# Kernel optimization log

Measured on AMD Instinct MI355X. Metric: run time of the kernel, lower is better.

## Reference

```python
import jax, jax.numpy as jnp
import numpy as np

B, N, T, D, H = 2, 1024, 12, 64, 4
HD = D // H


def _ln(x, g, b, eps=1e-5):
    m = x.mean(-1, keepdims=True)
    v = x.var(-1, keepdims=True)
    return (x - m) / jnp.sqrt(v + eps) * g + b


def setup_inputs() -> dict:
    key = jax.random.key(0)
    ks = jax.random.split(key, 12)
    s = 1.0 / np.sqrt(D)
    s4 = 1.0 / np.sqrt(4 * D)
    return {
        "x": jax.random.normal(ks[0], (B, N, T, D), jnp.float32),
        "adj": jax.random.randint(ks[1], (N, N), 0, 2, jnp.int32),
        "wq": jax.random.normal(ks[2], (D, D), jnp.float32) * s,
        "wk": jax.random.normal(ks[3], (D, D), jnp.float32) * s,
        "wv": jax.random.normal(ks[4], (D, D), jnp.float32) * s,
        "wo": jax.random.normal(ks[5], (D, D), jnp.float32) * s,
        "bo": jnp.zeros((D,), jnp.float32),
        "w1": jax.random.normal(ks[6], (D, 4 * D), jnp.float32) * s,
        "b1": jnp.zeros((4 * D,), jnp.float32),
        "w2": jax.random.normal(ks[7], (4 * D, D), jnp.float32) * s4,
        "b2": jnp.zeros((D,), jnp.float32),
        "g1": jnp.ones((D,), jnp.float32),
        "be1": jnp.zeros((D,), jnp.float32),
        "g2": jnp.ones((D,), jnp.float32),
        "be2": jnp.zeros((D,), jnp.float32),
    }


def reference(x, adj, wq, wk, wv, wo, bo, w1, b1, w2, b2, g1, be1, g2, be2):
    # x: [B, N, T, D]; all timesteps are independent -> vectorize over T.
    b, n, t, d = x.shape
    xt = x.transpose(0, 2, 1, 3)  # [B, T, N, D]
    h = _ln(xt, g1, be1)
    q = (h @ wq).reshape(b, t, n, H, HD)
    k = (h @ wk).reshape(b, t, n, H, HD)
    v = (h @ wv).reshape(b, t, n, H, HD)
    # scores: [B, T, H, N, N]
    scores = jnp.einsum("btihc,btjhc->bthij", q, k) / np.sqrt(HD)
    scores = jnp.where(adj[None, None, None] == 0, jnp.float32(-1e9), scores)
    attn = jax.nn.softmax(scores, axis=-1)
    o = jnp.einsum("bthij,btjhc->btihc", attn, v).reshape(b, t, n, d)
    xt = xt + (o @ wo + bo)
    h = _ln(xt, g2, be2)
    h = jax.nn.relu(h @ w1 + b1) @ w2 + b2
    xt = xt + h
    return xt.transpose(0, 2, 1, 3)  # [B, N, T, D]
```

## Files before the change

### kernel.cpp

```cpp
#include <hip/hip_runtime.h>
#include <hip/hip_bf16.h>

#define DEV __device__ __forceinline__

constexpr int Nn = 1024, Tn = 12, Dn = 64;

#if __has_builtin(__builtin_amdgcn_exp2f)
DEV float fast_exp2(float x) { return __builtin_amdgcn_exp2f(x); }
#else
DEV float fast_exp2(float x) { return exp2f(x); }
#endif

typedef __bf16 bf16x8 __attribute__((ext_vector_type(8)));
typedef float f32x4 __attribute__((ext_vector_type(4)));
typedef float f32x16 __attribute__((ext_vector_type(16)));

#define Z16 {0.f,0.f,0.f,0.f, 0.f,0.f,0.f,0.f, 0.f,0.f,0.f,0.f, 0.f,0.f,0.f,0.f}

DEV unsigned f2b(float f) {
  unsigned u = __builtin_bit_cast(unsigned, f);
  return (u + 0x8000u) >> 16;
}
DEV unsigned pk2(float a, float b) { return f2b(a) | (f2b(b) << 16); }
DEV float b2f(unsigned hbits) { return __builtin_bit_cast(float, hbits << 16); }
DEV void split2(float a, float b, unsigned& hw, unsigned& lw) {
  unsigned ha = f2b(a), hb = f2b(b);
  hw = ha | (hb << 16);
  lw = pk2(a - b2f(ha), b - b2f(hb));
}

DEV void wave_reduce2(float& s, float& s2) {
#pragma unroll
  for (int off = 32; off; off >>= 1) {
    s += __shfl_xor(s, off, 64);
    s2 += __shfl_xor(s2, off, 64);
  }
}

__global__ __launch_bounds__(256) void k_pack(const int* __restrict__ adj,
                                              unsigned long long* __restrict__ packed) {
  int gw = (blockIdx.x * 256 + threadIdx.x) >> 6;
  int lane = threadIdx.x & 63;
  int v = adj[(gw << 6) + lane];
  unsigned long long m = __ballot(v != 0);
  if (lane == 0) packed[gw] = m;
}

__global__ __launch_bounds__(256) void k_prep(
    const float* __restrict__ wo, const float* __restrict__ w1,
    const float* __restrict__ w2, const float* __restrict__ b1,
    const float* __restrict__ g2, const float* __restrict__ be2,
    __hip_bfloat16* __restrict__ woP, __hip_bfloat16* __restrict__ w1P,
    __hip_bfloat16* __restrict__ w2P, float* __restrict__ b1p) {
  int tid = blockIdx.x * 256 + threadIdx.x;
  if (tid < 512) {
    int fg = tid >> 6, lane = tid & 63;
    int t = fg >> 2, ks = fg & 3, hi = lane >> 5, l31 = lane & 31;
    unsigned hw[4], lw[4];
#pragma unroll
    for (int jj = 0; jj < 4; ++jj) {
      int k = ks * 16 + hi * 8 + jj * 2;
      split2(wo[k * 64 + t * 32 + l31], wo[(k + 1) * 64 + t * 32 + l31], hw[jj], lw[jj]);
    }
    *(uint4*)(woP + (size_t)tid * 8) = make_uint4(hw[0], hw[1], hw[2], hw[3]);
    *(uint4*)(woP + (size_t)(512 + tid) * 8) = make_uint4(lw[0], lw[1], lw[2], lw[3]);
  } else if (tid < 2560) {
    int id = tid - 512;
    int fg = id >> 6, lane = id & 63;
    int tile = fg >> 2, ks = fg & 3, hi = lane >> 5, l31 = lane & 31;
    unsigned hw[4], lw[4];
#pragma unroll
    for (int jj = 0; jj < 4; ++jj) {
      int k = ks * 16 + hi * 8 + jj * 2;
      split2(g2[k] * w1[k * 256 + tile * 32 + l31],
             g2[k + 1] * w1[(k + 1) * 256 + tile * 32 + l31], hw[jj], lw[jj]);
    }
    *(uint4*)(w1P + (size_t)id * 8) = make_uint4(hw[0], hw[1], hw[2], hw[3]);
    *(uint4*)(w1P + (size_t)(2048 + id) * 8) = make_uint4(lw[0], lw[1], lw[2], lw[3]);
  } else if (tid < 4608) {
    int id = tid - 2560;
    int fg = id >> 6, lane = id & 63;
    int t = fg >> 4, ks = fg & 15, hi = lane >> 5, l31 = lane & 31;
    unsigned hw[4], lw[4];
#pragma unroll
    for (int jj = 0; jj < 4; ++jj) {
      int k = ks * 16 + hi * 8 + jj * 2;
      split2(w2[k * 64 + t * 32 + l31], w2[(k + 1) * 64 + t * 32 + l31], hw[jj], lw[jj]);
    }
    *(uint4*)(w2P + (size_t)id * 8) = make_uint4(hw[0], hw[1], hw[2], hw[3]);
    *(uint4*)(w2P + (size_t)(2048 + id) * 8) = make_uint4(lw[0], lw[1], lw[2], lw[3]);
  } else if (tid < 4864) {
    int o = tid - 4608;
    float s = b1[o];
    for (int c = 0; c < 64; ++c) s += be2[c] * w1[c * 256 + o];
    b1p[o] = s;
  }
}

__global__ __launch_bounds__(256) void k_ln1_qkv(
    const float* __restrict__ x, const float* __restrict__ wq,
    const float* __restrict__ wk, const float* __restrict__ wv,
    const float* __restrict__ g1, const float* __restrict__ be1,
    __hip_bfloat16* __restrict__ Qb, __hip_bfloat16* __restrict__ Kb,
    __hip_bfloat16* __restrict__ Vt) {
  __shared__ float wlds[64 * 192];
  __shared__ float hlds[4][16][68];
  int tid = threadIdx.x, lane = tid & 63, w = tid >> 6;
  for (int i = tid * 4; i < 4096; i += 1024) {
    int c = i >> 6, d = i & 63;
    *(float4*)&wlds[c * 192 + d]       = *(const float4*)&wq[i];
    *(float4*)&wlds[c * 192 + 64 + d]  = *(const float4*)&wk[i];
    *(float4*)&wlds[c * 192 + 128 + d] = *(const float4*)&wv[i];
  }
  float g = g1[lane], be = be1[lane];
  __syncthreads();
  int row0 = blockIdx.x * 64 + w * 16;
  int bt = row0 >> 10, n0 = row0 & 1023;
#pragma unroll 1
  for (int r = 0; r < 16; ++r) {
    int n = n0 + r;
    int b = bt / Tn, t = bt - b * Tn;
    float xv = x[((b * Nn + n) * Tn + t) * 64 + lane];
    float s = xv, s2 = xv * xv;
    wave_reduce2(s, s2);
    float mean = s * 0.015625f;
    float var = s2 * 0.015625f - mean * mean;
    float rs = rsqrtf(var + 1e-5f);
    hlds[w][r][lane] = (xv - mean) * rs * g + be;
  }
  float qa[16], ka[16], va[16];
#pragma unroll
  for (int r = 0; r < 16; ++r) { qa[r] = 0.f; ka[r] = 0.f; va[r] = 0.f; }
  for (int c = 0; c < 64; c += 4) {
    float wq4[4], wk4[4], wv4[4];
#pragma unroll
    for (int cc = 0; cc < 4; ++cc) {
      wq4[cc] = wlds[(c + cc) * 192 + lane];
      wk4[cc] = wlds[(c + cc) * 192 + 64 + lane];
      wv4[cc] = wlds[(c + cc) * 192 + 128 + lane];
    }
#pragma unroll
    for (int r = 0; r < 16; ++r) {
      float4 h4 = *(float4*)&hlds[w][r][c];
      qa[r] = fmaf(h4.x, wq4[0], qa[r]); qa[r] = fmaf(h4.y, wq4[1], qa[r]);
      qa[r] = fmaf(h4.z, wq4[2], qa[r]); qa[r] = fmaf(h4.w, wq4[3], qa[r]);
      ka[r] = fmaf(h4.x, wk4[0], ka[r]); ka[r] = fmaf(h4.y, wk4[1], ka[r]);
      ka[r] = fmaf(h4.z, wk4[2], ka[r]); ka[r] = fmaf(h4.w, wk4[3], ka[r]);
      va[r] = fmaf(h4.x, wv4[0], va[r]); va[r] = fmaf(h4.y, wv4[1], va[r]);
      va[r] = fmaf(h4.z, wv4[2], va[r]); va[r] = fmaf(h4.w, wv4[3], va[r]);
    }
  }
  const float QS = 0.25f * 1.44269504088896f;
  int hh = lane >> 4, cc = lane & 15;
#pragma unroll 1
  for (int r = 0; r < 16; ++r) {
    int n = n0 + r;
    size_t idx = ((size_t)(bt * 4 + hh) * 1024 + n) * 16 + cc;
    Qb[idx] = __hip_bfloat16_raw{(unsigned short)f2b(qa[r] * QS)};
    Kb[idx] = __hip_bfloat16_raw{(unsigned short)f2b(ka[r])};
  }
#pragma unroll
  for (int r = 0; r < 16; ++r) hlds[w][r][lane] = va[r];
  unsigned os[8];
#pragma unroll
  for (int j = 0; j < 8; ++j)
    os[j] = f2b(hlds[w][2 * j][lane]) | (f2b(hlds[w][2 * j + 1][lane]) << 16);
  uint4* vo = (uint4*)(Vt + ((size_t)(bt * 4 + hh) * 16 + cc) * 1024 + n0);
  vo[0] = make_uint4(os[0], os[1], os[2], os[3]);
  vo[1] = make_uint4(os[4], os[5], os[6], os[7]);
}

__global__ __launch_bounds__(256) void k_attn(
    const __hip_bfloat16* __restrict__ Qb, const __hip_bfloat16* __restrict__ Kb,
    const __hip_bfloat16* __restrict__ Vt, const unsigned* __restrict__ packed32,
    float* __restrict__ O) {
  __shared__ uint4 smem[4][160];
  int bid = (blockIdx.x & 7) * 96 + (blockIdx.x >> 3);
  int bth = bid >> 3, qb = bid & 7;
  int bt = bth >> 2, h = bth & 3;
  int tid = threadIdx.x, lane = tid & 63, w = tid >> 6;
  int l15 = lane & 15, l31 = lane & 31, hi = lane >> 5, g4 = lane >> 4;
  int q0 = qb * 128 + w * 32;
  bf16x8 qfrag = __builtin_bit_cast(bf16x8,
      *(const uint4*)(Qb + ((size_t)bth * 1024 + q0 + l31) * 16 + hi * 8));
  const uint4* kbase = (const uint4*)(Kb + (size_t)bth * 1024 * 16);
  const uint4* vtb = (const uint4*)(Vt + (size_t)bth * 16 * 1024);
  const unsigned* mbase = packed32 + (size_t)(q0 + l31) * 32;
  char* myp = (char*)&smem[w][0];

  f32x4 o1 = {0.f, 0.f, 0.f, 0.f}, o2 = {0.f, 0.f, 0.f, 0.f};
  float m = -1e38f, lsum = 0.f;
  uint4 kf = kbase[l31 * 2 + hi];
  uint4 vf = vtb[l15 * 128 + g4];
  unsigned mk = mbase[0];
#pragma unroll 1
  for (int kt = 0; kt < 32; ++kt) {
    int ktn = kt < 31 ? kt + 1 : 31;
    uint4 kf_n = kbase[ktn * 64 + l31 * 2 + hi];
    uint4 vf_n = vtb[l15 * 128 + ktn * 4 + g4];
    unsigned mk_n = mbase[ktn];
    f32x16 s = Z16;
    s = __builtin_amdgcn_mfma_f32_32x32x16_bf16(
        __builtin_bit_cast(bf16x8, kf), qfrag, s, 0, 0, 0);
    unsigned mm = mk >> (hi * 4);
#pragma unroll
    for (int r = 0; r < 16; ++r)
      if (!((mm >> ((r & 3) + 8 * (r >> 2))) & 1u)) s[r] = -3e38f;
    float tm = s[0];
#pragma unroll
    for (int r = 1; r < 16; ++r) tm = fmaxf(tm, s[r]);
    tm = fmaxf(tm, __shfl_xor(tm, 32));
    float mn = fmaxf(m, tm);
    float sc = fast_exp2(m - mn);
    m = mn;
    lsum *= sc;
    float sc1 = __shfl(sc, l15), sc2 = __shfl(sc, l15 + 16);
#pragma unroll
    for (int r = 0; r < 4; ++r) { o1[r] *= sc1; o2[r] *= sc2; }
    float p[16];
#pragma unroll
    for (int r = 0; r < 16; ++r) { p[r] = fast_exp2(s[r] - m); lsum += p[r]; }
    unsigned pw[8];
#pragma unroll
    for (int j = 0; j < 8; ++j) pw[j] = pk2(p[2 * j], p[2 * j + 1]);
    char* wp = myp + l31 * 80 + hi * 8;
    *(uint2*)(wp +  0) = make_uint2(pw[0], pw[1]);
    *(uint2*)(wp + 16) = make_uint2(pw[2], pw[3]);
    *(uint2*)(wp + 32) = make_uint2(pw[4], pw[5]);
    *(uint2*)(wp + 48) = make_uint2(pw[6], pw[7]);
    uint4 b1v = *(uint4*)(myp + l15 * 80 + g4 * 16);
    uint4 b2v = *(uint4*)(myp + (l15 + 16) * 80 + g4 * 16);
    bf16x8 vfrag = __builtin_bit_cast(bf16x8, vf);
    o1 = __builtin_amdgcn_mfma_f32_16x16x32_bf16(
        vfrag, __builtin_bit_cast(bf16x8, b1v), o1, 0, 0, 0);
    o2 = __builtin_amdgcn_mfma_f32_16x16x32_bf16(
        vfrag, __builtin_bit_cast(bf16x8, b2v), o2, 0, 0, 0);
    kf = kf_n; vf = vf_n; mk = mk_n;
  }
  float lt = lsum + __shfl_xor(lsum, 32);
  float inv = lt > 0.f ? 1.f / lt : 0.f;
  float inv1 = __shfl(inv, l15), inv2 = __shfl(inv, l15 + 16);
  float* of = (float*)myp;
#pragma unroll
  for (int r = 0; r < 4; ++r) {
    of[l15 * 20 + g4 * 4 + r] = o1[r] * inv1;
    of[(l15 + 16) * 20 + g4 * 4 + r] = o2[r] * inv2;
  }
  float* orow = O + ((size_t)bt * 1024 + q0 + l31) * 64 + h * 16 + hi * 8;
  *(float4*)(orow)     = *(float4*)(myp + l31 * 80 + hi * 32);
  *(float4*)(orow + 4) = *(float4*)(myp + l31 * 80 + hi * 32 + 16);
}

__global__ __launch_bounds__(64) void k_tail(
    const float* __restrict__ O, const float* __restrict__ x,
    const __hip_bfloat16* __restrict__ woP, const __hip_bfloat16* __restrict__ w1P,
    const __hip_bfloat16* __restrict__ w2P, const float* __restrict__ bo,
    const float* __restrict__ b1p, const float* __restrict__ b2,
    float* __restrict__ out) {
  __shared__ float bias[384];
  __shared__ char wbuf[13312];
  int lane = threadIdx.x & 63;
  int l31 = lane & 31, hi = lane >> 5;
  for (int i = threadIdx.x; i < 384; i += 64)
    bias[i] = i < 64 ? bo[i] : (i < 128 ? b2[i - 64] : b1p[i - 128]);
  __syncthreads();

  int tok = blockIdx.x * 32 + l31;
  int bt = tok >> 10, n = tok & 1023;
  int b = bt / Tn, tt_time = bt - b * Tn;
  const float* orow = O + (size_t)tok * 64;
  const float* xrow = x + ((size_t)(b * Nn + n) * Tn + tt_time) * 64;
  char* h2b = wbuf;
  char* pub = wbuf + 8704;

#define LDA(base, g) __builtin_bit_cast(bf16x8, *(const uint4*)((base) + ((size_t)(g) * 64 + lane) * 8))
#define MF(A, B, C) __builtin_amdgcn_mfma_f32_32x32x16_bf16(A, B, C, 0, 0, 0)

  bf16x8 ofh[4], ofl[4];
#pragma unroll
  for (int ks = 0; ks < 4; ++ks) {
    float4 oa = *(const float4*)(orow + ks * 16 + hi * 8);
    float4 ob = *(const float4*)(orow + ks * 16 + hi * 8 + 4);
    unsigned hw[4], lw[4];
    split2(oa.x, oa.y, hw[0], lw[0]); split2(oa.z, oa.w, hw[1], lw[1]);
    split2(ob.x, ob.y, hw[2], lw[2]); split2(ob.z, ob.w, hw[3], lw[3]);
    ofh[ks] = __builtin_bit_cast(bf16x8, make_uint4(hw[0], hw[1], hw[2], hw[3]));
    ofl[ks] = __builtin_bit_cast(bf16x8, make_uint4(lw[0], lw[1], lw[2], lw[3]));
  }
  f32x16 d1a = Z16, d1b = Z16;
#pragma unroll
  for (int ks = 0; ks < 4; ++ks) {
    bf16x8 wha = LDA(woP, ks), wla = LDA(woP, 8 + ks);
    d1a = MF(wha, ofh[ks], d1a); d1a = MF(wha, ofl[ks], d1a); d1a = MF(wla, ofh[ks], d1a);
    bf16x8 whb = LDA(woP, 4 + ks), wlb = LDA(woP, 12 + ks);
    d1b = MF(whb, ofh[ks], d1b); d1b = MF(whb, ofl[ks], d1b); d1b = MF(wlb, ofh[ks], d1b);
  }
#pragma unroll
  for (int rq = 0; rq < 4; ++rq) {
    float4 xa = *(const float4*)(xrow + rq * 8 + hi * 4);
    float4 xb = *(const float4*)(xrow + 32 + rq * 8 + hi * 4);
    int ca = rq * 8 + hi * 4, cb = 32 + rq * 8 + hi * 4;
    d1a[rq * 4 + 0] += bias[ca + 0] + xa.x;  d1a[rq * 4 + 1] += bias[ca + 1] + xa.y;
    d1a[rq * 4 + 2] += bias[ca + 2] + xa.z;  d1a[rq * 4 + 3] += bias[ca + 3] + xa.w;
    d1b[rq * 4 + 0] += bias[cb + 0] + xb.x;  d1b[rq * 4 + 1] += bias[cb + 1] + xb.y;
    d1b[rq * 4 + 2] += bias[cb + 2] + xb.z;  d1b[rq * 4 + 3] += bias[cb + 3] + xb.w;
  }
  float s = 0.f, s2 = 0.f;
#pragma unroll
  for (int r = 0; r < 16; ++r) {
    s += d1a[r] + d1b[r];
    s2 += d1a[r] * d1a[r] + d1b[r] * d1b[r];
  }
  s += __shfl_xor(s, 32);  s2 += __shfl_xor(s2, 32);
  float mean = s * 0.015625f;
  float rs = rsqrtf(s2 * 0.015625f - mean * mean + 1e-5f);
#pragma unroll
  for (int rq = 0; rq < 4; ++rq) {
    unsigned h0, l0, h1, l1;
    split2((d1a[rq * 4 + 0] - mean) * rs, (d1a[rq * 4 + 1] - mean) * rs, h0, l0);
    split2((d1a[rq * 4 + 2] - mean) * rs, (d1a[rq * 4 + 3] - mean) * rs, h1, l1);
    *(uint2*)(h2b + l31 * 272 + rq * 16 + hi * 8) = make_uint2(h0, h1);
    *(uint2*)(h2b + l31 * 272 + 128 + rq * 16 + hi * 8) = make_uint2(l0, l1);
    split2((d1b[rq * 4 + 0] - mean) * rs, (d1b[rq * 4 + 1] - mean) * rs, h0, l0);
    split2((d1b[rq * 4 + 2] - mean) * rs, (d1b[rq * 4 + 3] - mean) * rs, h1, l1);
    *(uint2*)(h2b + l31 * 272 + 64 + rq * 16 + hi * 8) = make_uint2(h0, h1);
    *(uint2*)(h2b + l31 * 272 + 192 + rq * 16 + hi * 8) = make_uint2(l0, l1);
  }
  bf16x8 hfh[4], hfl[4];
#pragma unroll
  for (int ks = 0; ks < 4; ++ks) {
    hfh[ks] = __builtin_bit_cast(bf16x8, *(const uint4*)(h2b + l31 * 272 + ks * 32 + hi * 16));
    hfl[ks] = __builtin_bit_cast(bf16x8, *(const uint4*)(h2b + l31 * 272 + 128 + ks * 32 + hi * 16));
  }
  f32x16 d3a = Z16, d3b = Z16;
#pragma unroll 1
  for (int tt = 0; tt < 8; ++tt) {
    f32x16 u = Z16;
#pragma unroll
    for (int ks = 0; ks < 4; ++ks) {
      bf16x8 wh = LDA(w1P, tt * 4 + ks), wl = LDA(w1P, 32 + tt * 4 + ks);
      u = MF(wh, hfh[ks], u); u = MF(wh, hfl[ks], u); u = MF(wl, hfh[ks], u);
    }
#pragma unroll
    for (int r = 0; r < 16; ++r) {
      int ch = tt * 32 + (r & 3) + 8 * (r >> 2) + 4 * hi;
      u[r] = fmaxf(u[r] + bias[128 + ch], 0.f);
    }
#pragma unroll
    for (int rq = 0; rq < 4; ++rq) {
      unsigned h0, l0, h1, l1;
      split2(u[rq * 4 + 0], u[rq * 4 + 1], h0, l0);
      split2(u[rq * 4 + 2], u[rq * 4 + 3], h1, l1);
      *(uint2*)(pub + l31 * 144 + rq * 16 + hi * 8) = make_uint2(h0, h1);
      *(uint2*)(pub + l31 * 144 + 64 + rq * 16 + hi * 8) = make_uint2(l0, l1);
    }
    bf16x8 uh0 = __builtin_bit_cast(bf16x8, *(const uint4*)(pub + l31 * 144 + hi * 16));
    bf16x8 uh1 = __builtin_bit_cast(bf16x8, *(const uint4*)(pub + l31 * 144 + 32 + hi * 16));
    bf16x8 ul0 = __builtin_bit_cast(bf16x8, *(const uint4*)(pub + l31 * 144 + 64 + hi * 16));
    bf16x8 ul1 = __builtin_bit_cast(bf16x8, *(const uint4*)(pub + l31 * 144 + 96 + hi * 16));
    bf16x8 w2h0 = LDA(w2P, tt * 2),      w2h1 = LDA(w2P, tt * 2 + 1);
    bf16x8 w2l0 = LDA(w2P, 32 + tt * 2), w2l1 = LDA(w2P, 32 + tt * 2 + 1);
    d3a = MF(w2h0, uh0, d3a); d3a = MF(w2h0, ul0, d3a); d3a = MF(w2l0, uh0, d3a);
    d3a = MF(w2h1, uh1, d3a); d3a = MF(w2h1, ul1, d3a); d3a = MF(w2l1, uh1, d3a);
    bf16x8 w2h2 = LDA(w2P, 16 + tt * 2),      w2h3 = LDA(w2P, 16 + tt * 2 + 1);
    bf16x8 w2l2 = LDA(w2P, 48 + tt * 2),      w2l3 = LDA(w2P, 48 + tt * 2 + 1);
    d3b = MF(w2h2, uh0, d3b); d3b = MF(w2h2, ul0, d3b); d3b = MF(w2l2, uh0, d3b);
    d3b = MF(w2h3, uh1, d3b); d3b = MF(w2h3, ul1, d3b); d3b = MF(w2l3, uh1, d3b);
  }
#pragma unroll
  for (int rq = 0; rq < 4; ++rq) {
    int ca = rq * 8 + hi * 4, cb = 32 + rq * 8 + hi * 4;
    float4 va, vb;
    va.x = d3a[rq * 4 + 0] + bias[64 + ca + 0] + d1a[rq * 4 + 0];
    va.y = d3a[rq * 4 + 1] + bias[64 + ca + 1] + d1a[rq * 4 + 1];
    va.z = d3a[rq * 4 + 2] + bias[64 + ca + 2] + d1a[rq * 4 + 2];
    va.w = d3a[rq * 4 + 3] + bias[64 + ca + 3] + d1a[rq * 4 + 3];
    vb.x = d3b[rq * 4 + 0] + bias[64 + cb + 0] + d1b[rq * 4 + 0];
    vb.y = d3b[rq * 4 + 1] + bias[64 + cb + 1] + d1b[rq * 4 + 1];
    vb.z = d3b[rq * 4 + 2] + bias[64 + cb + 2] + d1b[rq * 4 + 2];
    vb.w = d3b[rq * 4 + 3] + bias[64 + cb + 3] + d1b[rq * 4 + 3];
    *(float4*)(h2b + l31 * 272 + rq * 32 + hi * 16) = va;
    *(float4*)(h2b + l31 * 272 + 128 + rq * 32 + hi * 16) = vb;
  }
  float* gout = out + ((size_t)(b * Nn + n) * Tn + tt_time) * 64 + hi * 32;
#pragma unroll
  for (int i = 0; i < 8; ++i)
    *(float4*)(gout + i * 4) = *(float4*)(h2b + l31 * 272 + hi * 128 + i * 16);
#undef LDA
#undef MF
}

extern "C" void kernel_launch(void* const* d_in, const int* in_sizes, int n_in,
                              void* d_out, int out_size, void* d_ws, size_t ws_size,
                              hipStream_t stream) {
  const float* x   = (const float*)d_in[0];
  const int* adj   = (const int*)d_in[1];
  const float* wq  = (const float*)d_in[2];
  const float* wk  = (const float*)d_in[3];
  const float* wv  = (const float*)d_in[4];
  const float* wo  = (const float*)d_in[5];
  const float* bo  = (const float*)d_in[6];
  const float* w1  = (const float*)d_in[7];
  const float* b1  = (const float*)d_in[8];
  const float* w2  = (const float*)d_in[9];
  const float* b2  = (const float*)d_in[10];
  const float* g1  = (const float*)d_in[11];
  const float* be1 = (const float*)d_in[12];
  const float* g2  = (const float*)d_in[13];
  const float* be2 = (const float*)d_in[14];
  float* out = (float*)d_out;

  float* ws = (float*)d_ws;
  unsigned long long* packed = (unsigned long long*)ws;
  __hip_bfloat16* Qb = (__hip_bfloat16*)(ws + 32768);
  __hip_bfloat16* Kb = (__hip_bfloat16*)(ws + 819200);
  __hip_bfloat16* Vt = (__hip_bfloat16*)(ws + 1605632);
  float* O = ws + 2392064;
  __hip_bfloat16* woP = (__hip_bfloat16*)(ws + 3964928);
  __hip_bfloat16* w1P = (__hip_bfloat16*)(ws + 3969024);
  __hip_bfloat16* w2P = (__hip_bfloat16*)(ws + 3985408);
  float* b1p = ws + 4001792;

  k_pack<<<4096, 256, 0, stream>>>(adj, packed);
  k_prep<<<19, 256, 0, stream>>>(wo, w1, w2, b1, g2, be2, woP, w1P, w2P, b1p);
  k_ln1_qkv<<<384, 256, 0, stream>>>(x, wq, wk, wv, g1, be1, Qb, Kb, Vt);
  k_attn<<<768, 256, 0, stream>>>(Qb, Kb, Vt, (const unsigned*)packed, O);
  k_tail<<<768, 64, 0, stream>>>(O, x, woP, w1P, w2P, bo, b1p, b2, out);
}
```

Before: 180.3 us.

## Precompute additive mask bias tiles and apply lazy softmax rescaling in attention

A new k_bias kernel expands the packed adjacency bits into per-tile float bias fragments (0 or -1e30) laid out to match the MFMA accumulator. The attention kernel then uses them as the initial accumulator, which removes the per-element bit tests and selects. It also skips the online-softmax rescale unless the running max grows by more than 8 in log2 units, uses native bf16 conversion for P, and shrinks the LDS row stride from 80 to 72 bytes. The cost is a 4 MB bias tensor in fp32 that each attention block streams from memory, instead of a 4-byte mask word per row per tile, plus one extra kernel launch.

```diff
diff --git a/kernel.cpp b/kernel.cpp
--- a/kernel.cpp
+++ b/kernel.cpp
@@ -12,6 +12,7 @@
 #endif
 
 typedef __bf16 bf16x8 __attribute__((ext_vector_type(8)));
+typedef __bf16 bf16x2 __attribute__((ext_vector_type(2)));
 typedef float f32x4 __attribute__((ext_vector_type(4)));
 typedef float f32x16 __attribute__((ext_vector_type(16)));
 
@@ -44,6 +45,25 @@
   int v = adj[(gw << 6) + lane];
   unsigned long long m = __ballot(v != 0);
   if (lane == 0) packed[gw] = m;
+}
+
+__global__ __launch_bounds__(256) void k_bias(const unsigned* __restrict__ packed32,
+                                              float* __restrict__ biasF) {
+  int tid = blockIdx.x * 256 + threadIdx.x;
+  int tile = tid >> 6, lane = tid & 63;
+  int qb32 = tile >> 5, kt = tile & 31;
+  int l31 = lane & 31, hi = lane >> 5;
+  unsigned mm = packed32[(size_t)(qb32 * 32 + l31) * 32 + kt] >> (hi * 4);
+  float* base = biasF + (size_t)tile * 1024 + lane * 4;
+#pragma unroll
+  for (int c = 0; c < 4; ++c) {
+    float4 v;
+    v.x = ((mm >> (((c * 4 + 0) & 3) + 8 * ((c * 4 + 0) >> 2))) & 1u) ? 0.f : -1e30f;
+    v.y = ((mm >> (((c * 4 + 1) & 3) + 8 * ((c * 4 + 1) >> 2))) & 1u) ? 0.f : -1e30f;
+    v.z = ((mm >> (((c * 4 + 2) & 3) + 8 * ((c * 4 + 2) >> 2))) & 1u) ? 0.f : -1e30f;
+    v.w = ((mm >> (((c * 4 + 3) & 3) + 8 * ((c * 4 + 3) >> 2))) & 1u) ? 0.f : -1e30f;
+    *(float4*)(base + c * 256) = v;
+  }
 }
 
 __global__ __launch_bounds__(256) void k_prep(
@@ -172,7 +192,7 @@
 
 __global__ __launch_bounds__(256) void k_attn(
     const __hip_bfloat16* __restrict__ Qb, const __hip_bfloat16* __restrict__ Kb,
-    const __hip_bfloat16* __restrict__ Vt, const unsigned* __restrict__ packed32,
+    const __hip_bfloat16* __restrict__ Vt, const float* __restrict__ biasF,
     float* __restrict__ O) {
   __shared__ uint4 smem[4][160];
   int bid = (blockIdx.x & 7) * 96 + (blockIdx.x >> 3);
@@ -185,57 +205,70 @@
       *(const uint4*)(Qb + ((size_t)bth * 1024 + q0 + l31) * 16 + hi * 8));
   const uint4* kbase = (const uint4*)(Kb + (size_t)bth * 1024 * 16);
   const uint4* vtb = (const uint4*)(Vt + (size_t)bth * 16 * 1024);
-  const unsigned* mbase = packed32 + (size_t)(q0 + l31) * 32;
+  const float* bbase = biasF + ((size_t)(qb * 4 + w) * 32) * 1024 + lane * 4;
   char* myp = (char*)&smem[w][0];
 
   f32x4 o1 = {0.f, 0.f, 0.f, 0.f}, o2 = {0.f, 0.f, 0.f, 0.f};
-  float m = -1e38f, lsum = 0.f;
+  float m = -3e38f, lsum = 0.f;
   uint4 kf = kbase[l31 * 2 + hi];
   uint4 vf = vtb[l15 * 128 + g4];
-  unsigned mk = mbase[0];
+  f32x4 bf0 = *(const f32x4*)(bbase + 0);
+  f32x4 bf1 = *(const f32x4*)(bbase + 256);
+  f32x4 bf2 = *(const f32x4*)(bbase + 512);
+  f32x4 bf3 = *(const f32x4*)(bbase + 768);
 #pragma unroll 1
   for (int kt = 0; kt < 32; ++kt) {
     int ktn = kt < 31 ? kt + 1 : 31;
     uint4 kf_n = kbase[ktn * 64 + l31 * 2 + hi];
     uint4 vf_n = vtb[l15 * 128 + ktn * 4 + g4];
-    unsigned mk_n = mbase[ktn];
-    f32x16 s = Z16;
+    const float* bbn = bbase + (size_t)ktn * 1024;
+    f32x4 bn0 = *(const f32x4*)(bbn + 0);
+    f32x4 bn1 = *(const f32x4*)(bbn + 256);
+    f32x4 bn2 = *(const f32x4*)(bbn + 512);
+    f32x4 bn3 = *(const f32x4*)(bbn + 768);
+    f32x16 s = {bf0.x, bf0.y, bf0.z, bf0.w, bf1.x, bf1.y, bf1.z, bf1.w,
+                bf2.x, bf2.y, bf2.z, bf2.w, bf3.x, bf3.y, bf3.z, bf3.w};
     s = __builtin_amdgcn_mfma_f32_32x32x16_bf16(
         __builtin_bit_cast(bf16x8, kf), qfrag, s, 0, 0, 0);
-    unsigned mm = mk >> (hi * 4);
-#pragma unroll
-    for (int r = 0; r < 16; ++r)
-      if (!((mm >> ((r & 3) + 8 * (r >> 2))) & 1u)) s[r] = -3e38f;
-    float tm = s[0];
-#pragma unroll
-    for (int r = 1; r < 16; ++r) tm = fmaxf(tm, s[r]);
+    float t0 = fmaxf(fmaxf(s[0], s[1]), s[2]);
+    float t1 = fmaxf(fmaxf(s[3], s[4]), s[5]);
+    float t2 = fmaxf(fmaxf(s[6], s[7]), s[8]);
+    float t3 = fmaxf(fmaxf(s[9], s[10]), s[11]);
+    float t4 = fmaxf(fmaxf(s[12], s[13]), s[14]);
+    float tm = fmaxf(fmaxf(fmaxf(t0, t1), t2), fmaxf(fmaxf(t3, t4), s[15]));
     tm = fmaxf(tm, __shfl_xor(tm, 32));
     float mn = fmaxf(m, tm);
-    float sc = fast_exp2(m - mn);
-    m = mn;
-    lsum *= sc;
-    float sc1 = __shfl(sc, l15), sc2 = __shfl(sc, l15 + 16);
-#pragma unroll
-    for (int r = 0; r < 4; ++r) { o1[r] *= sc1; o2[r] *= sc2; }
+    if (!__all(mn <= m + 8.f)) {
+      float sc = fast_exp2(m - mn);
+      m = mn;
+      lsum *= sc;
+      float sc1 = __shfl(sc, l15), sc2 = __shfl(sc, l15 + 16);
+#pragma unroll
+      for (int r = 0; r < 4; ++r) { o1[r] *= sc1; o2[r] *= sc2; }
+    }
     float p[16];
 #pragma unroll
     for (int r = 0; r < 16; ++r) { p[r] = fast_exp2(s[r] - m); lsum += p[r]; }
     unsigned pw[8];
 #pragma unroll
-    for (int j = 0; j < 8; ++j) pw[j] = pk2(p[2 * j], p[2 * j + 1]);
-    char* wp = myp + l31 * 80 + hi * 8;
+    for (int j = 0; j < 8; ++j) {
+      bf16x2 t = {(__bf16)p[2 * j], (__bf16)p[2 * j + 1]};
+      pw[j] = __builtin_bit_cast(unsigned, t);
+    }
+    char* wp = myp + l31 * 72 + hi * 8;
     *(uint2*)(wp +  0) = make_uint2(pw[0], pw[1]);
     *(uint2*)(wp + 16) = make_uint2(pw[2], pw[3]);
     *(uint2*)(wp + 32) = make_uint2(pw[4], pw[5]);
     *(uint2*)(wp + 48) = make_uint2(pw[6], pw[7]);
-    uint4 b1v = *(uint4*)(myp + l15 * 80 + g4 * 16);
-    uint4 b2v = *(uint4*)(myp + (l15 + 16) * 80 + g4 * 16);
+    uint4 b1v = *(uint4*)(myp + l15 * 72 + g4 * 16);
+    uint4 b2v = *(uint4*)(myp + (l15 + 16) * 72 + g4 * 16);
     bf16x8 vfrag = __builtin_bit_cast(bf16x8, vf);
     o1 = __builtin_amdgcn_mfma_f32_16x16x32_bf16(
         vfrag, __builtin_bit_cast(bf16x8, b1v), o1, 0, 0, 0);
     o2 = __builtin_amdgcn_mfma_f32_16x16x32_bf16(
         vfrag, __builtin_bit_cast(bf16x8, b2v), o2, 0, 0, 0);
-    kf = kf_n; vf = vf_n; mk = mk_n;
+    kf = kf_n; vf = vf_n;
+    bf0 = bn0; bf1 = bn1; bf2 = bn2; bf3 = bn3;
   }
   float lt = lsum + __shfl_xor(lsum, 32);
   float inv = lt > 0.f ? 1.f / lt : 0.f;
@@ -420,10 +453,12 @@
   __hip_bfloat16* w1P = (__hip_bfloat16*)(ws + 3969024);
   __hip_bfloat16* w2P = (__hip_bfloat16*)(ws + 3985408);
   float* b1p = ws + 4001792;
+  float* biasF = ws + 4002048;
 
   k_pack<<<4096, 256, 0, stream>>>(adj, packed);
+  k_bias<<<256, 256, 0, stream>>>((const unsigned*)packed, biasF);
   k_prep<<<19, 256, 0, stream>>>(wo, w1, w2, b1, g2, be2, woP, w1P, w2P, b1p);
   k_ln1_qkv<<<384, 256, 0, stream>>>(x, wq, wk, wv, g1, be1, Qb, Kb, Vt);
-  k_attn<<<768, 256, 0, stream>>>(Qb, Kb, Vt, (const unsigned*)packed, O);
+  k_attn<<<768, 256, 0, stream>>>(Qb, Kb, Vt, biasF, O);
   k_tail<<<768, 64, 0, stream>>>(O, x, woP, w1P, w2P, bo, b1p, b2, out);
 }
```

After: 175.2 us. 2.8% less time.
